# Kernel optimization log

Measured on AMD Instinct MI355X. Metric: run time of the kernel, lower is better.

## Reference

```python
import jax, jax.numpy as jnp
import numpy as np

N_NODES = 10000
N_EDGES = 320000
D_IN = 256
D_OUT = 256
NEG_SLOPE = 0.2


def setup_inputs() -> dict:
    key = jax.random.key(0)
    ks = jax.random.split(key, 8)
    feature = jax.random.normal(ks[0], (N_NODES, D_IN), dtype=jnp.float32)
    src = jax.random.randint(ks[1], (N_EDGES,), 0, N_NODES, dtype=jnp.int32)
    dst = jax.random.randint(ks[2], (N_EDGES,), 0, N_NODES, dtype=jnp.int32)
    # Xavier-ish scaled weights
    s = 1.0 / np.sqrt(D_IN)
    W_s = jax.random.normal(ks[3], (D_OUT, D_IN), dtype=jnp.float32) * s
    W_t = jax.random.normal(ks[4], (D_OUT, D_IN), dtype=jnp.float32) * s
    W_attn = jax.random.normal(ks[5], (1, D_OUT), dtype=jnp.float32) * (1.0 / np.sqrt(D_OUT))
    W_fc = jax.random.normal(ks[6], (D_OUT, D_IN), dtype=jnp.float32) * s
    b_fc = jnp.zeros((D_OUT,), dtype=jnp.float32)
    return {"feature": feature, "src": src, "dst": dst,
            "W_s": W_s, "W_t": W_t, "W_attn": W_attn,
            "W_fc": W_fc, "b_fc": b_fc}


def reference(feature, src, dst, W_s, W_t, W_attn, W_fc, b_fc):
    n = feature.shape[0]
    # Project at node level, then gather (same math as projecting gathered feats).
    proj_s = feature @ W_s.T          # [N, D_OUT]
    proj_t = feature @ W_t.T          # [N, D_OUT]
    # Edge attention logits: attn(LeakyReLU(h_dst + h_src))
    z = proj_s[src] + proj_t[dst]     # [E, D_OUT]
    z = jnp.where(z >= 0, z, NEG_SLOPE * z)
    e = (z @ W_attn.T)[:, 0]          # [E]
    # edge_softmax with norm_by='src': softmax over outgoing edges of each src node
    m = jax.ops.segment_max(e, src, num_segments=n)          # [N]
    m = jnp.where(jnp.isfinite(m), m, 0.0)                   # guard empty segments
    e_exp = jnp.exp(e - m[src])                               # [E]
    denom = jax.ops.segment_sum(e_exp, src, num_segments=n)  # [N]
    alpha = e_exp / denom[src]                                # [E]
    # message = src feature * alpha; reduce = sum at dst
    msg = feature[src] * alpha[:, None]                       # [E, D_IN]
    agg = jax.ops.segment_sum(msg, dst, num_segments=n)       # [N, D_IN]
    # final linear
    return agg @ W_fc.T + b_fc
```

## Files before the change

### kernel.cpp

```cpp
#include <hip/hip_runtime.h>
#include <math.h>

#define N_NODES 10000
#define N_EDGES 320000
#define D 256
#define NEG_SLOPE 0.2f
#define BCAP 96
#define BLOCK 256
#define NF4 (N_NODES * D / 4)
#define NW4 (256 * 256 / 4)
#define NTILE_M 157
#define NTILES (NTILE_M * 12)
#define FILL_BLOCKS ((N_EDGES + BLOCK - 1) / BLOCK)
#define CPAD 66

typedef unsigned short ushortT;
typedef __attribute__((ext_vector_type(8))) short bf16x8;
typedef __attribute__((ext_vector_type(4))) float f32x4;

__device__ __forceinline__ unsigned short f2bf(float f) {
  unsigned int u = __float_as_uint(f);
  u += 0x7FFFu + ((u >> 16) & 1u);
  return (unsigned short)(u >> 16);
}
__device__ __forceinline__ float bf2f(unsigned short u) {
  return __uint_as_float((unsigned int)u << 16);
}

typedef const __attribute__((address_space(1))) unsigned int* gas_ptr;
typedef __attribute__((address_space(3))) unsigned int* las_ptr;
__device__ __forceinline__ void gload16(const void* g, void* l) {
  __builtin_amdgcn_global_load_lds((gas_ptr)g, (las_ptr)l, 16, 0, 0);
}

__global__ void prep_kernel(const float* __restrict__ feat,
                            const float* __restrict__ Ws,
                            const float* __restrict__ Wt,
                            const float* __restrict__ Wfc,
                            ushortT* __restrict__ featb,
                            ushortT* __restrict__ Wcat,
                            int* __restrict__ cnt,
                            float* __restrict__ denom) {
  const int g = blockIdx.x * blockDim.x + threadIdx.x;
  if (g < NF4) {
    float4 v = ((const float4*)feat)[g];
    ushort4 u;
    u.x = f2bf(v.x); u.y = f2bf(v.y); u.z = f2bf(v.z); u.w = f2bf(v.w);
    ((ushort4*)featb)[g] = u;
    return;
  }
  const int gi = g - NF4;
  if (gi < 3 * NW4) {
    const float* W = (gi < NW4) ? Ws : ((gi < 2 * NW4) ? Wt : Wfc);
    const int off = gi - ((gi < NW4) ? 0 : ((gi < 2 * NW4) ? NW4 : 2 * NW4));
    float4 v = ((const float4*)W)[off];
    ushort4 u;
    u.x = f2bf(v.x); u.y = f2bf(v.y); u.z = f2bf(v.z); u.w = f2bf(v.w);
    ((ushort4*)Wcat)[gi] = u;
    return;
  }
  const int gn = gi - 3 * NW4;
  if (gn < N_NODES) {
    cnt[gn] = 0;
    denom[gn] = 0.f;
  }
}

__global__ __launch_bounds__(256, 2) void proj_fill_kernel(
    const ushortT* __restrict__ featb,
    const ushortT* __restrict__ Wcat,
    const int* __restrict__ src, const int* __restrict__ dst,
    int* __restrict__ cnt, int* __restrict__ src_b,
    ushortT* __restrict__ ps, ushortT* __restrict__ pt,
    ushortT* __restrict__ fcp) {
  __shared__ ushortT Als[64][D];
  __shared__ ushortT Bls[64][D];
  __shared__ ushortT Cls[64][CPAD];

  if (blockIdx.x < FILL_BLOCKS) {
    const int i = blockIdx.x * BLOCK + threadIdx.x;
    if (i < N_EDGES) {
      const int dn = dst[i];
      const int slot = atomicAdd(&cnt[dn], 1);
      if (slot < BCAP) src_b[dn * BCAP + slot] = src[i];
    }
    return;
  }
  const int p = blockIdx.x - FILL_BLOCKS;
  const int m0 = (p / 12) * 64;
  const int by = p % 12;
  ushortT* outp = (by < 4) ? ps : ((by < 8) ? pt : fcp);
  const int col0 = (by & 3) * 64;
  const int n0 = by * 64;

  const int tid = threadIdx.x;
  const int wave = tid >> 6;
  const int lane = tid & 63;
  const int quad = lane >> 4;
  const int l16 = lane & 15;

  const int m_base_t = (wave & 1) * 32;
  const int wn = wave >> 1;

  {
    const int rl = lane >> 5;
    const int cph = lane & 31;
#pragma unroll
    for (int c = 0; c < 8; ++c) {
      const int r = wave * 16 + c * 2 + rl;
      const int clog = cph ^ (r & 7);
      gload16(featb + (size_t)(m0 + r) * D + clog * 8, &Als[wave * 16 + c * 2][0]);
      gload16(Wcat + (size_t)(n0 + r) * D + clog * 8, &Bls[wave * 16 + c * 2][0]);
    }
  }
  __syncthreads();

  f32x4 acc[2][2];
#pragma unroll
  for (int i = 0; i < 2; ++i)
#pragma unroll
    for (int j = 0; j < 2; ++j) acc[i][j] = (f32x4){0.f, 0.f, 0.f, 0.f};

  const int ar0 = m_base_t + l16;
  const int br0 = wn * 32 + l16;
  const int xa = ar0 & 7;
  const int xb = br0 & 7;
#pragma unroll
  for (int kk = 0; kk < 8; ++kk) {
    const int j = kk * 4 + quad;
    const int ea = (j ^ xa) * 8;
    const int eb = (j ^ xb) * 8;
    bf16x8 a0 = *(const bf16x8*)&Als[ar0][ea];
    bf16x8 a1 = *(const bf16x8*)&Als[ar0 + 16][ea];
    bf16x8 b0 = *(const bf16x8*)&Bls[br0][eb];
    bf16x8 b1 = *(const bf16x8*)&Bls[br0 + 16][eb];
    acc[0][0] = __builtin_amdgcn_mfma_f32_16x16x32_bf16(a0, b0, acc[0][0], 0, 0, 0);
    acc[0][1] = __builtin_amdgcn_mfma_f32_16x16x32_bf16(a0, b1, acc[0][1], 0, 0, 0);
    acc[1][0] = __builtin_amdgcn_mfma_f32_16x16x32_bf16(a1, b0, acc[1][0], 0, 0, 0);
    acc[1][1] = __builtin_amdgcn_mfma_f32_16x16x32_bf16(a1, b1, acc[1][1], 0, 0, 0);
  }

#pragma unroll
  for (int mi = 0; mi < 2; ++mi)
#pragma unroll
    for (int r = 0; r < 4; ++r) {
      const int row = m_base_t + mi * 16 + quad * 4 + r;
#pragma unroll
      for (int ni = 0; ni < 2; ++ni)
        Cls[row][wn * 32 + ni * 16 + l16] = f2bf(acc[mi][ni][r]);
    }
  __syncthreads();
#pragma unroll
  for (int it = 0; it < 2; ++it) {
    const int idx = tid + it * 256;
    const int row = idx >> 3;
    const int cc = (idx & 7) * 8;
    const int grow = m0 + row;
    if (grow < N_NODES)
      *(bf16x8*)(outp + (size_t)grow * D + col0 + cc) = *(const bf16x8*)&Cls[row][cc];
  }
}

__global__ __launch_bounds__(256) void logit_bucket_kernel(
    const ushortT* __restrict__ ps,
    const ushortT* __restrict__ pt,
    const int* __restrict__ cnt,
    const int* __restrict__ src_b,
    const float* __restrict__ Wattn,
    float* __restrict__ expv_b,
    float* __restrict__ denom) {
  const int wave = threadIdx.x >> 6;
  const int n = blockIdx.x * 4 + wave;
  if (n >= N_NODES) return;
  const int cn = min(cnt[n], BCAP);
  if (cn == 0) return;
  const int lane = threadIdx.x & 63;
  const int half = lane >> 5;
  const int l32 = lane & 31;
  const int base = n * BCAP;

  bf16x8 bu = *(const bf16x8*)(pt + (size_t)n * D + l32 * 8);
  float b[8], w[8];
  const float4 w0 = *(const float4*)(Wattn + l32 * 8);
  const float4 w1 = *(const float4*)(Wattn + l32 * 8 + 4);
  w[0] = w0.x; w[1] = w0.y; w[2] = w0.z; w[3] = w0.w;
  w[4] = w1.x; w[5] = w1.y; w[6] = w1.z; w[7] = w1.w;
#pragma unroll
  for (int i = 0; i < 8; ++i) b[i] = bf2f((unsigned short)bu[i]);

  int j = half;
  for (; j + 6 < cn; j += 8) {
    const int s0 = src_b[base + j];
    const int s1 = src_b[base + j + 2];
    const int s2 = src_b[base + j + 4];
    const int s3 = src_b[base + j + 6];
    bf16x8 au0 = *(const bf16x8*)(ps + (size_t)s0 * D + l32 * 8);
    bf16x8 au1 = *(const bf16x8*)(ps + (size_t)s1 * D + l32 * 8);
    bf16x8 au2 = *(const bf16x8*)(ps + (size_t)s2 * D + l32 * 8);
    bf16x8 au3 = *(const bf16x8*)(ps + (size_t)s3 * D + l32 * 8);
    float sum0 = 0.f, sum1 = 0.f, sum2 = 0.f, sum3 = 0.f;
#pragma unroll
    for (int i = 0; i < 8; ++i) {
      float z0 = bf2f((unsigned short)au0[i]) + b[i];
      float z1 = bf2f((unsigned short)au1[i]) + b[i];
      float z2 = bf2f((unsigned short)au2[i]) + b[i];
      float z3 = bf2f((unsigned short)au3[i]) + b[i];
      z0 = fmaxf(z0, NEG_SLOPE * z0);
      z1 = fmaxf(z1, NEG_SLOPE * z1);
      z2 = fmaxf(z2, NEG_SLOPE * z2);
      z3 = fmaxf(z3, NEG_SLOPE * z3);
      sum0 = fmaf(w[i], z0, sum0);
      sum1 = fmaf(w[i], z1, sum1);
      sum2 = fmaf(w[i], z2, sum2);
      sum3 = fmaf(w[i], z3, sum3);
    }
#pragma unroll
    for (int off = 16; off > 0; off >>= 1) {
      sum0 += __shfl_down(sum0, off, 32);
      sum1 += __shfl_down(sum1, off, 32);
      sum2 += __shfl_down(sum2, off, 32);
      sum3 += __shfl_down(sum3, off, 32);
    }
    if (l32 == 0) {
      float ex0 = __expf(sum0), ex1 = __expf(sum1);
      float ex2 = __expf(sum2), ex3 = __expf(sum3);
      expv_b[base + j] = ex0;
      expv_b[base + j + 2] = ex1;
      expv_b[base + j + 4] = ex2;
      expv_b[base + j + 6] = ex3;
      atomicAdd(&denom[s0], ex0);
      atomicAdd(&denom[s1], ex1);
      atomicAdd(&denom[s2], ex2);
      atomicAdd(&denom[s3], ex3);
    }
  }
  for (; j < cn; j += 2) {
    const int s = src_b[base + j];
    bf16x8 au = *(const bf16x8*)(ps + (size_t)s * D + l32 * 8);
    float sum = 0.f;
#pragma unroll
    for (int i = 0; i < 8; ++i) {
      float z = bf2f((unsigned short)au[i]) + b[i];
      z = fmaxf(z, NEG_SLOPE * z);
      sum = fmaf(w[i], z, sum);
    }
#pragma unroll
    for (int off = 16; off > 0; off >>= 1) sum += __shfl_down(sum, off, 32);
    if (l32 == 0) {
      float ex = __expf(sum);
      expv_b[base + j] = ex;
      atomicAdd(&denom[s], ex);
    }
  }
}

__global__ __launch_bounds__(256) void gather_agg_kernel(
    const ushortT* __restrict__ fcp,
    const int* __restrict__ cnt,
    const int* __restrict__ src_b,
    const float* __restrict__ expv_b,
    const float* __restrict__ denom,
    const float* __restrict__ b_fc,
    float* __restrict__ out) {
  const int wave = threadIdx.x >> 6;
  const int n = blockIdx.x * 4 + wave;
  if (n >= N_NODES) return;
  const int lane = threadIdx.x & 63;
  const int half = lane >> 5;
  const int l32 = lane & 31;
  const int cn = min(cnt[n], BCAP);
  const int base = n * BCAP;

  float acc[8];
#pragma unroll
  for (int i = 0; i < 8; ++i) acc[i] = 0.f;

  int j = half;
  for (; j + 6 < cn; j += 8) {
    const int s0 = src_b[base + j];
    const int s1 = src_b[base + j + 2];
    const int s2 = src_b[base + j + 4];
    const int s3 = src_b[base + j + 6];
    const float a0 = expv_b[base + j] / denom[s0];
    const float a1 = expv_b[base + j + 2] / denom[s1];
    const float a2 = expv_b[base + j + 4] / denom[s2];
    const float a3 = expv_b[base + j + 6] / denom[s3];
    bf16x8 f0 = *(const bf16x8*)(fcp + (size_t)s0 * D + l32 * 8);
    bf16x8 f1 = *(const bf16x8*)(fcp + (size_t)s1 * D + l32 * 8);
    bf16x8 f2 = *(const bf16x8*)(fcp + (size_t)s2 * D + l32 * 8);
    bf16x8 f3 = *(const bf16x8*)(fcp + (size_t)s3 * D + l32 * 8);
#pragma unroll
    for (int i = 0; i < 8; ++i) {
      acc[i] = fmaf(a0, bf2f((unsigned short)f0[i]), acc[i]);
      acc[i] = fmaf(a1, bf2f((unsigned short)f1[i]), acc[i]);
      acc[i] = fmaf(a2, bf2f((unsigned short)f2[i]), acc[i]);
      acc[i] = fmaf(a3, bf2f((unsigned short)f3[i]), acc[i]);
    }
  }
  for (; j < cn; j += 2) {
    const int s = src_b[base + j];
    const float a = expv_b[base + j] / denom[s];
    bf16x8 fu = *(const bf16x8*)(fcp + (size_t)s * D + l32 * 8);
#pragma unroll
    for (int i = 0; i < 8; ++i)
      acc[i] = fmaf(a, bf2f((unsigned short)fu[i]), acc[i]);
  }
#pragma unroll
  for (int i = 0; i < 8; ++i) acc[i] += __shfl_xor(acc[i], 32);
  if (half == 0) {
    const float4 bf0 = *(const float4*)(b_fc + l32 * 8);
    const float4 bf1 = *(const float4*)(b_fc + l32 * 8 + 4);
    float4 o0 = make_float4(acc[0] + bf0.x, acc[1] + bf0.y, acc[2] + bf0.z, acc[3] + bf0.w);
    float4 o1 = make_float4(acc[4] + bf1.x, acc[5] + bf1.y, acc[6] + bf1.z, acc[7] + bf1.w);
    *(float4*)(out + (size_t)n * D + l32 * 8) = o0;
    *(float4*)(out + (size_t)n * D + l32 * 8 + 4) = o1;
  }
}

extern "C" void kernel_launch(void* const* d_in, const int* in_sizes, int n_in,
                              void* d_out, int out_size, void* d_ws, size_t ws_size,
                              hipStream_t stream) {
  const float* feat  = (const float*)d_in[0];
  const int*   src   = (const int*)d_in[1];
  const int*   dst   = (const int*)d_in[2];
  const float* Ws    = (const float*)d_in[3];
  const float* Wt    = (const float*)d_in[4];
  const float* Wattn = (const float*)d_in[5];
  const float* Wfc   = (const float*)d_in[6];
  const float* bfc   = (const float*)d_in[7];
  float* out = (float*)d_out;

  ushortT* ps    = (ushortT*)d_ws;
  ushortT* pt    = ps + (size_t)N_NODES * D;
  ushortT* fcp   = pt + (size_t)N_NODES * D;
  ushortT* featb = fcp + (size_t)N_NODES * D;
  ushortT* Wcat  = featb + (size_t)N_NODES * D;
  float* expv_b  = (float*)(Wcat + (size_t)768 * 256);
  float* denom   = expv_b + (size_t)N_NODES * BCAP;
  int*   cnt     = (int*)(denom + N_NODES);
  int*   src_b   = cnt + N_NODES;

  const int prep_items = NF4 + 3 * NW4 + N_NODES;
  const int nodeblocks = (N_NODES + 3) / 4;
  prep_kernel<<<(prep_items + BLOCK - 1) / BLOCK, BLOCK, 0, stream>>>(
      feat, Ws, Wt, Wfc, featb, Wcat, cnt, denom);
  proj_fill_kernel<<<FILL_BLOCKS + NTILES, BLOCK, 0, stream>>>(
      featb, Wcat, src, dst, cnt, src_b, ps, pt, fcp);
  logit_bucket_kernel<<<nodeblocks, BLOCK, 0, stream>>>(ps, pt, cnt, src_b, Wattn, expv_b, denom);
  gather_agg_kernel<<<nodeblocks, BLOCK, 0, stream>>>(fcp, cnt, src_b, expv_b, denom, bfc, out);
}
```

Baseline: 162.1 us.

## Quantize gathered projection rows to int8 with per-row scales

```diff
diff --git a/kernel.cpp b/kernel.cpp
--- a/kernel.cpp
+++ b/kernel.cpp
@@ -25,6 +25,9 @@
 }
 __device__ __forceinline__ float bf2f(unsigned short u) {
   return __uint_as_float((unsigned int)u << 16);
+}
+__device__ __forceinline__ float i8get(int w, int i) {
+  return (float)((signed char)(w >> (8 * i)));
 }
 
 typedef const __attribute__((address_space(1))) unsigned int* gas_ptr;
@@ -161,8 +164,37 @@
   }
 }
 
+__global__ __launch_bounds__(256) void quant_kernel(
+    const ushortT* __restrict__ ps, const ushortT* __restrict__ fcp,
+    signed char* __restrict__ ps8, signed char* __restrict__ fcp8,
+    float* __restrict__ sps, float* __restrict__ sfcp) {
+  const int wid = blockIdx.x * 4 + (threadIdx.x >> 6);
+  if (wid >= 2 * N_NODES) return;
+  const int lane = threadIdx.x & 63;
+  const bool isPs = (wid < N_NODES);
+  const int row = isPs ? wid : wid - N_NODES;
+  const ushortT* sp = isPs ? ps : fcp;
+  signed char* dp = isPs ? ps8 : fcp8;
+  float* scp = isPs ? sps : sfcp;
+
+  ushort4 u = *(const ushort4*)(sp + (size_t)row * D + lane * 4);
+  float v0 = bf2f(u.x), v1 = bf2f(u.y), v2 = bf2f(u.z), v3 = bf2f(u.w);
+  float m = fmaxf(fmaxf(fabsf(v0), fabsf(v1)), fmaxf(fabsf(v2), fabsf(v3)));
+#pragma unroll
+  for (int off = 32; off > 0; off >>= 1) m = fmaxf(m, __shfl_xor(m, off));
+  const float rs = (m > 0.f) ? 127.f / m : 0.f;
+  const int q0 = (int)rintf(v0 * rs);
+  const int q1 = (int)rintf(v1 * rs);
+  const int q2 = (int)rintf(v2 * rs);
+  const int q3 = (int)rintf(v3 * rs);
+  const int packed = (q0 & 255) | ((q1 & 255) << 8) | ((q2 & 255) << 16) | (q3 << 24);
+  ((int*)dp)[row * 64 + lane] = packed;
+  if (lane == 0) scp[row] = m * (1.f / 127.f);
+}
+
 __global__ __launch_bounds__(256) void logit_bucket_kernel(
-    const ushortT* __restrict__ ps,
+    const signed char* __restrict__ ps8,
+    const float* __restrict__ sps,
     const ushortT* __restrict__ pt,
     const int* __restrict__ cnt,
     const int* __restrict__ src_b,
@@ -194,17 +226,23 @@
     const int s1 = src_b[base + j + 2];
     const int s2 = src_b[base + j + 4];
     const int s3 = src_b[base + j + 6];
-    bf16x8 au0 = *(const bf16x8*)(ps + (size_t)s0 * D + l32 * 8);
-    bf16x8 au1 = *(const bf16x8*)(ps + (size_t)s1 * D + l32 * 8);
-    bf16x8 au2 = *(const bf16x8*)(ps + (size_t)s2 * D + l32 * 8);
-    bf16x8 au3 = *(const bf16x8*)(ps + (size_t)s3 * D + l32 * 8);
+    const int2 q0 = *(const int2*)(ps8 + (size_t)s0 * D + l32 * 8);
+    const int2 q1 = *(const int2*)(ps8 + (size_t)s1 * D + l32 * 8);
+    const int2 q2 = *(const int2*)(ps8 + (size_t)s2 * D + l32 * 8);
+    const int2 q3 = *(const int2*)(ps8 + (size_t)s3 * D + l32 * 8);
+    const float c0 = sps[s0], c1 = sps[s1], c2 = sps[s2], c3 = sps[s3];
     float sum0 = 0.f, sum1 = 0.f, sum2 = 0.f, sum3 = 0.f;
 #pragma unroll
     for (int i = 0; i < 8; ++i) {
-      float z0 = bf2f((unsigned short)au0[i]) + b[i];
-      float z1 = bf2f((unsigned short)au1[i]) + b[i];
-      float z2 = bf2f((unsigned short)au2[i]) + b[i];
-      float z3 = bf2f((unsigned short)au3[i]) + b[i];
+      const int w0q = (i < 4) ? q0.x : q0.y;
+      const int w1q = (i < 4) ? q1.x : q1.y;
+      const int w2q = (i < 4) ? q2.x : q2.y;
+      const int w3q = (i < 4) ? q3.x : q3.y;
+      const int bi = i & 3;
+      float z0 = fmaf(i8get(w0q, bi), c0, b[i]);
+      float z1 = fmaf(i8get(w1q, bi), c1, b[i]);
+      float z2 = fmaf(i8get(w2q, bi), c2, b[i]);
+      float z3 = fmaf(i8get(w3q, bi), c3, b[i]);
       z0 = fmaxf(z0, NEG_SLOPE * z0);
       z1 = fmaxf(z1, NEG_SLOPE * z1);
       z2 = fmaxf(z2, NEG_SLOPE * z2);
@@ -236,11 +274,13 @@
   }
   for (; j < cn; j += 2) {
     const int s = src_b[base + j];
-    bf16x8 au = *(const bf16x8*)(ps + (size_t)s * D + l32 * 8);
+    const int2 q = *(const int2*)(ps8 + (size_t)s * D + l32 * 8);
+    const float c = sps[s];
     float sum = 0.f;
 #pragma unroll
     for (int i = 0; i < 8; ++i) {
-      float z = bf2f((unsigned short)au[i]) + b[i];
+      const int wq = (i < 4) ? q.x : q.y;
+      float z = fmaf(i8get(wq, i & 3), c, b[i]);
       z = fmaxf(z, NEG_SLOPE * z);
       sum = fmaf(w[i], z, sum);
     }
@@ -255,7 +295,8 @@
 }
 
 __global__ __launch_bounds__(256) void gather_agg_kernel(
-    const ushortT* __restrict__ fcp,
+    const signed char* __restrict__ fcp8,
+    const float* __restrict__ sfcp,
     const int* __restrict__ cnt,
     const int* __restrict__ src_b,
     const float* __restrict__ expv_b,
@@ -281,29 +322,30 @@
     const int s1 = src_b[base + j + 2];
     const int s2 = src_b[base + j + 4];
     const int s3 = src_b[base + j + 6];
-    const float a0 = expv_b[base + j] / denom[s0];
-    const float a1 = expv_b[base + j + 2] / denom[s1];
-    const float a2 = expv_b[base + j + 4] / denom[s2];
-    const float a3 = expv_b[base + j + 6] / denom[s3];
-    bf16x8 f0 = *(const bf16x8*)(fcp + (size_t)s0 * D + l32 * 8);
-    bf16x8 f1 = *(const bf16x8*)(fcp + (size_t)s1 * D + l32 * 8);
-    bf16x8 f2 = *(const bf16x8*)(fcp + (size_t)s2 * D + l32 * 8);
-    bf16x8 f3 = *(const bf16x8*)(fcp + (size_t)s3 * D + l32 * 8);
+    const float a0 = expv_b[base + j] / denom[s0] * sfcp[s0];
+    const float a1 = expv_b[base + j + 2] / denom[s1] * sfcp[s1];
+    const float a2 = expv_b[base + j + 4] / denom[s2] * sfcp[s2];
+    const float a3 = expv_b[base + j + 6] / denom[s3] * sfcp[s3];
+    const int2 q0 = *(const int2*)(fcp8 + (size_t)s0 * D + l32 * 8);
+    const int2 q1 = *(const int2*)(fcp8 + (size_t)s1 * D + l32 * 8);
+    const int2 q2 = *(const int2*)(fcp8 + (size_t)s2 * D + l32 * 8);
+    const int2 q3 = *(const int2*)(fcp8 + (size_t)s3 * D + l32 * 8);
 #pragma unroll
     for (int i = 0; i < 8; ++i) {
-      acc[i] = fmaf(a0, bf2f((unsigned short)f0[i]), acc[i]);
-      acc[i] = fmaf(a1, bf2f((unsigned short)f1[i]), acc[i]);
-      acc[i] = fmaf(a2, bf2f((unsigned short)f2[i]), acc[i]);
-      acc[i] = fmaf(a3, bf2f((unsigned short)f3[i]), acc[i]);
+      const int bi = i & 3;
+      acc[i] = fmaf(a0, i8get((i < 4) ? q0.x : q0.y, bi), acc[i]);
+      acc[i] = fmaf(a1, i8get((i < 4) ? q1.x : q1.y, bi), acc[i]);
+      acc[i] = fmaf(a2, i8get((i < 4) ? q2.x : q2.y, bi), acc[i]);
+      acc[i] = fmaf(a3, i8get((i < 4) ? q3.x : q3.y, bi), acc[i]);
     }
   }
   for (; j < cn; j += 2) {
     const int s = src_b[base + j];
-    const float a = expv_b[base + j] / denom[s];
-    bf16x8 fu = *(const bf16x8*)(fcp + (size_t)s * D + l32 * 8);
+    const float a = expv_b[base + j] / denom[s] * sfcp[s];
+    const int2 q = *(const int2*)(fcp8 + (size_t)s * D + l32 * 8);
 #pragma unroll
     for (int i = 0; i < 8; ++i)
-      acc[i] = fmaf(a, bf2f((unsigned short)fu[i]), acc[i]);
+      acc[i] = fmaf(a, i8get((i < 4) ? q.x : q.y, i & 3), acc[i]);
   }
 #pragma unroll
   for (int i = 0; i < 8; ++i) acc[i] += __shfl_xor(acc[i], 32);
@@ -339,6 +381,10 @@
   float* denom   = expv_b + (size_t)N_NODES * BCAP;
   int*   cnt     = (int*)(denom + N_NODES);
   int*   src_b   = cnt + N_NODES;
+  signed char* ps8  = (signed char*)(src_b + (size_t)N_NODES * BCAP);
+  signed char* fcp8 = ps8 + (size_t)N_NODES * D;
+  float* sps     = (float*)(fcp8 + (size_t)N_NODES * D);
+  float* sfcp    = sps + N_NODES;
 
   const int prep_items = NF4 + 3 * NW4 + N_NODES;
   const int nodeblocks = (N_NODES + 3) / 4;
@@ -346,6 +392,7 @@
       feat, Ws, Wt, Wfc, featb, Wcat, cnt, denom);
   proj_fill_kernel<<<FILL_BLOCKS + NTILES, BLOCK, 0, stream>>>(
       featb, Wcat, src, dst, cnt, src_b, ps, pt, fcp);
-  logit_bucket_kernel<<<nodeblocks, BLOCK, 0, stream>>>(ps, pt, cnt, src_b, Wattn, expv_b, denom);
-  gather_agg_kernel<<<nodeblocks, BLOCK, 0, stream>>>(fcp, cnt, src_b, expv_b, denom, bfc, out);
-}
+  quant_kernel<<<(2 * N_NODES + 3) / 4, BLOCK, 0, stream>>>(ps, fcp, ps8, fcp8, sps, sfcp);
+  logit_bucket_kernel<<<nodeblocks, BLOCK, 0, stream>>>(ps8, sps, pt, cnt, src_b, Wattn, expv_b, denom);
+  gather_agg_kernel<<<nodeblocks, BLOCK, 0, stream>>>(fcp8, sfcp, cnt, src_b, expv_b, denom, bfc, out);
+}
```

Result: slower. 166.7 us (+2.8%).

## Merge four kernels into one persistent cooperative kernel with grid syncs

Applied to the files above, without the earlier changes.

```diff
diff --git a/kernel.cpp b/kernel.cpp
--- a/kernel.cpp
+++ b/kernel.cpp
@@ -1,5 +1,8 @@
 #include <hip/hip_runtime.h>
+#include <hip/hip_cooperative_groups.h>
 #include <math.h>
+
+namespace cg = cooperative_groups;
 
 #define N_NODES 10000
 #define N_EDGES 320000
@@ -11,8 +14,8 @@
 #define NW4 (256 * 256 / 4)
 #define NTILE_M 157
 #define NTILES (NTILE_M * 12)
-#define FILL_BLOCKS ((N_EDGES + BLOCK - 1) / BLOCK)
 #define CPAD 66
+#define PREP_ITEMS (NF4 + 3 * NW4 + N_NODES)
 
 typedef unsigned short ushortT;
 typedef __attribute__((ext_vector_type(8))) short bf16x8;
@@ -33,287 +36,274 @@
   __builtin_amdgcn_global_load_lds((gas_ptr)g, (las_ptr)l, 16, 0, 0);
 }
 
-__global__ void prep_kernel(const float* __restrict__ feat,
-                            const float* __restrict__ Ws,
-                            const float* __restrict__ Wt,
-                            const float* __restrict__ Wfc,
-                            ushortT* __restrict__ featb,
-                            ushortT* __restrict__ Wcat,
-                            int* __restrict__ cnt,
-                            float* __restrict__ denom) {
-  const int g = blockIdx.x * blockDim.x + threadIdx.x;
-  if (g < NF4) {
-    float4 v = ((const float4*)feat)[g];
-    ushort4 u;
-    u.x = f2bf(v.x); u.y = f2bf(v.y); u.z = f2bf(v.z); u.w = f2bf(v.w);
-    ((ushort4*)featb)[g] = u;
-    return;
-  }
-  const int gi = g - NF4;
-  if (gi < 3 * NW4) {
-    const float* W = (gi < NW4) ? Ws : ((gi < 2 * NW4) ? Wt : Wfc);
-    const int off = gi - ((gi < NW4) ? 0 : ((gi < 2 * NW4) ? NW4 : 2 * NW4));
-    float4 v = ((const float4*)W)[off];
-    ushort4 u;
-    u.x = f2bf(v.x); u.y = f2bf(v.y); u.z = f2bf(v.z); u.w = f2bf(v.w);
-    ((ushort4*)Wcat)[gi] = u;
-    return;
-  }
-  const int gn = gi - 3 * NW4;
-  if (gn < N_NODES) {
-    cnt[gn] = 0;
-    denom[gn] = 0.f;
-  }
-}
-
-__global__ __launch_bounds__(256, 2) void proj_fill_kernel(
-    const ushortT* __restrict__ featb,
-    const ushortT* __restrict__ Wcat,
-    const int* __restrict__ src, const int* __restrict__ dst,
-    int* __restrict__ cnt, int* __restrict__ src_b,
+__global__ __launch_bounds__(256, 2) void mega_kernel(
+    const float* __restrict__ feat, const int* __restrict__ src,
+    const int* __restrict__ dst, const float* __restrict__ Ws,
+    const float* __restrict__ Wt, const float* __restrict__ Wattn,
+    const float* __restrict__ Wfc, const float* __restrict__ bfc,
+    ushortT* __restrict__ featb, ushortT* __restrict__ Wcat,
     ushortT* __restrict__ ps, ushortT* __restrict__ pt,
-    ushortT* __restrict__ fcp) {
+    ushortT* __restrict__ fcp, float* __restrict__ expv_b,
+    float* __restrict__ denom, int* __restrict__ cnt,
+    int* __restrict__ src_b, float* __restrict__ out) {
   __shared__ ushortT Als[64][D];
   __shared__ ushortT Bls[64][D];
   __shared__ ushortT Cls[64][CPAD];
 
-  if (blockIdx.x < FILL_BLOCKS) {
-    const int i = blockIdx.x * BLOCK + threadIdx.x;
-    if (i < N_EDGES) {
-      const int dn = dst[i];
-      const int slot = atomicAdd(&cnt[dn], 1);
-      if (slot < BCAP) src_b[dn * BCAP + slot] = src[i];
+  cg::grid_group grid = cg::this_grid();
+  const int tid = threadIdx.x;
+  const int gtid = blockIdx.x * BLOCK + tid;
+  const int gthreads = gridDim.x * BLOCK;
+
+  for (int g = gtid; g < PREP_ITEMS; g += gthreads) {
+    if (g < NF4) {
+      float4 v = ((const float4*)feat)[g];
+      ushort4 u;
+      u.x = f2bf(v.x); u.y = f2bf(v.y); u.z = f2bf(v.z); u.w = f2bf(v.w);
+      ((ushort4*)featb)[g] = u;
+    } else {
+      const int gi = g - NF4;
+      if (gi < 3 * NW4) {
+        const float* W = (gi < NW4) ? Ws : ((gi < 2 * NW4) ? Wt : Wfc);
+        const int off = gi - ((gi < NW4) ? 0 : ((gi < 2 * NW4) ? NW4 : 2 * NW4));
+        float4 v = ((const float4*)W)[off];
+        ushort4 u;
+        u.x = f2bf(v.x); u.y = f2bf(v.y); u.z = f2bf(v.z); u.w = f2bf(v.w);
+        ((ushort4*)Wcat)[gi] = u;
+      } else {
+        const int gn = gi - 3 * NW4;
+        if (gn < N_NODES) { cnt[gn] = 0; denom[gn] = 0.f; }
+      }
     }
-    return;
-  }
-  const int p = blockIdx.x - FILL_BLOCKS;
-  const int m0 = (p / 12) * 64;
-  const int by = p % 12;
-  ushortT* outp = (by < 4) ? ps : ((by < 8) ? pt : fcp);
-  const int col0 = (by & 3) * 64;
-  const int n0 = by * 64;
-
-  const int tid = threadIdx.x;
-  const int wave = tid >> 6;
-  const int lane = tid & 63;
-  const int quad = lane >> 4;
-  const int l16 = lane & 15;
-
-  const int m_base_t = (wave & 1) * 32;
-  const int wn = wave >> 1;
-
+  }
+  __threadfence();
+  grid.sync();
+
+  for (int i = gtid; i < N_EDGES; i += gthreads) {
+    const int dn = dst[i];
+    const int slot = atomicAdd(&cnt[dn], 1);
+    if (slot < BCAP) src_b[dn * BCAP + slot] = src[i];
+  }
   {
+    const int wave = tid >> 6;
+    const int lane = tid & 63;
+    const int quad = lane >> 4;
+    const int l16 = lane & 15;
+    const int m_base_t = (wave & 1) * 32;
+    const int wn = wave >> 1;
     const int rl = lane >> 5;
     const int cph = lane & 31;
-#pragma unroll
-    for (int c = 0; c < 8; ++c) {
-      const int r = wave * 16 + c * 2 + rl;
-      const int clog = cph ^ (r & 7);
-      gload16(featb + (size_t)(m0 + r) * D + clog * 8, &Als[wave * 16 + c * 2][0]);
-      gload16(Wcat + (size_t)(n0 + r) * D + clog * 8, &Bls[wave * 16 + c * 2][0]);
+    const int ar0 = m_base_t + l16;
+    const int br0 = wn * 32 + l16;
+    const int xa = ar0 & 7;
+    const int xb = br0 & 7;
+
+    for (int p = blockIdx.x; p < NTILES; p += gridDim.x) {
+      const int m0 = (p / 12) * 64;
+      const int by = p % 12;
+      ushortT* outp = (by < 4) ? ps : ((by < 8) ? pt : fcp);
+      const int col0 = (by & 3) * 64;
+      const int n0 = by * 64;
+
+#pragma unroll
+      for (int c = 0; c < 8; ++c) {
+        const int r = wave * 16 + c * 2 + rl;
+        const int clog = cph ^ (r & 7);
+        gload16(featb + (size_t)(m0 + r) * D + clog * 8, &Als[wave * 16 + c * 2][0]);
+        gload16(Wcat + (size_t)(n0 + r) * D + clog * 8, &Bls[wave * 16 + c * 2][0]);
+      }
+      __syncthreads();
+
+      f32x4 acc[2][2];
+#pragma unroll
+      for (int i2 = 0; i2 < 2; ++i2)
+#pragma unroll
+        for (int j2 = 0; j2 < 2; ++j2) acc[i2][j2] = (f32x4){0.f, 0.f, 0.f, 0.f};
+
+#pragma unroll
+      for (int kk = 0; kk < 8; ++kk) {
+        const int j = kk * 4 + quad;
+        const int ea = (j ^ xa) * 8;
+        const int eb = (j ^ xb) * 8;
+        bf16x8 a0 = *(const bf16x8*)&Als[ar0][ea];
+        bf16x8 a1 = *(const bf16x8*)&Als[ar0 + 16][ea];
+        bf16x8 b0 = *(const bf16x8*)&Bls[br0][eb];
+        bf16x8 b1 = *(const bf16x8*)&Bls[br0 + 16][eb];
+        acc[0][0] = __builtin_amdgcn_mfma_f32_16x16x32_bf16(a0, b0, acc[0][0], 0, 0, 0);
+        acc[0][1] = __builtin_amdgcn_mfma_f32_16x16x32_bf16(a0, b1, acc[0][1], 0, 0, 0);
+        acc[1][0] = __builtin_amdgcn_mfma_f32_16x16x32_bf16(a1, b0, acc[1][0], 0, 0, 0);
+        acc[1][1] = __builtin_amdgcn_mfma_f32_16x16x32_bf16(a1, b1, acc[1][1], 0, 0, 0);
+      }
+
+#pragma unroll
+      for (int mi = 0; mi < 2; ++mi)
+#pragma unroll
+        for (int r = 0; r < 4; ++r) {
+          const int row = m_base_t + mi * 16 + quad * 4 + r;
+#pragma unroll
+          for (int ni = 0; ni < 2; ++ni)
+            Cls[row][wn * 32 + ni * 16 + l16] = f2bf(acc[mi][ni][r]);
+        }
+      __syncthreads();
+#pragma unroll
+      for (int it = 0; it < 2; ++it) {
+        const int idx = tid + it * 256;
+        const int row = idx >> 3;
+        const int cc = (idx & 7) * 8;
+        const int grow = m0 + row;
+        if (grow < N_NODES)
+          *(bf16x8*)(outp + (size_t)grow * D + col0 + cc) = *(const bf16x8*)&Cls[row][cc];
+      }
     }
   }
-  __syncthreads();
-
-  f32x4 acc[2][2];
-#pragma unroll
-  for (int i = 0; i < 2; ++i)
-#pragma unroll
-    for (int j = 0; j < 2; ++j) acc[i][j] = (f32x4){0.f, 0.f, 0.f, 0.f};
-
-  const int ar0 = m_base_t + l16;
-  const int br0 = wn * 32 + l16;
-  const int xa = ar0 & 7;
-  const int xb = br0 & 7;
-#pragma unroll
-  for (int kk = 0; kk < 8; ++kk) {
-    const int j = kk * 4 + quad;
-    const int ea = (j ^ xa) * 8;
-    const int eb = (j ^ xb) * 8;
-    bf16x8 a0 = *(const bf16x8*)&Als[ar0][ea];
-    bf16x8 a1 = *(const bf16x8*)&Als[ar0 + 16][ea];
-    bf16x8 b0 = *(const bf16x8*)&Bls[br0][eb];
-    bf16x8 b1 = *(const bf16x8*)&Bls[br0 + 16][eb];
-    acc[0][0] = __builtin_amdgcn_mfma_f32_16x16x32_bf16(a0, b0, acc[0][0], 0, 0, 0);
-    acc[0][1] = __builtin_amdgcn_mfma_f32_16x16x32_bf16(a0, b1, acc[0][1], 0, 0, 0);
-    acc[1][0] = __builtin_amdgcn_mfma_f32_16x16x32_bf16(a1, b0, acc[1][0], 0, 0, 0);
-    acc[1][1] = __builtin_amdgcn_mfma_f32_16x16x32_bf16(a1, b1, acc[1][1], 0, 0, 0);
-  }
-
-#pragma unroll
-  for (int mi = 0; mi < 2; ++mi)
-#pragma unroll
-    for (int r = 0; r < 4; ++r) {
-      const int row = m_base_t + mi * 16 + quad * 4 + r;
-#pragma unroll
-      for (int ni = 0; ni < 2; ++ni)
-        Cls[row][wn * 32 + ni * 16 + l16] = f2bf(acc[mi][ni][r]);
+  __threadfence();
+  grid.sync();
+
+  {
+    const int gwave = gtid >> 6;
+    const int nwaves = gthreads >> 6;
+    const int lane = tid & 63;
+    const int half = lane >> 5;
+    const int l32 = lane & 31;
+    float w[8];
+    const float4 w0 = *(const float4*)(Wattn + l32 * 8);
+    const float4 w1 = *(const float4*)(Wattn + l32 * 8 + 4);
+    w[0] = w0.x; w[1] = w0.y; w[2] = w0.z; w[3] = w0.w;
+    w[4] = w1.x; w[5] = w1.y; w[6] = w1.z; w[7] = w1.w;
+
+    for (int n = gwave; n < N_NODES; n += nwaves) {
+      const int cn = min(cnt[n], BCAP);
+      if (cn == 0) continue;
+      const int base = n * BCAP;
+      bf16x8 bu = *(const bf16x8*)(pt + (size_t)n * D + l32 * 8);
+      float b[8];
+#pragma unroll
+      for (int i = 0; i < 8; ++i) b[i] = bf2f((unsigned short)bu[i]);
+
+      int j = half;
+      for (; j + 6 < cn; j += 8) {
+        const int s0 = src_b[base + j];
+        const int s1 = src_b[base + j + 2];
+        const int s2 = src_b[base + j + 4];
+        const int s3 = src_b[base + j + 6];
+        bf16x8 au0 = *(const bf16x8*)(ps + (size_t)s0 * D + l32 * 8);
+        bf16x8 au1 = *(const bf16x8*)(ps + (size_t)s1 * D + l32 * 8);
+        bf16x8 au2 = *(const bf16x8*)(ps + (size_t)s2 * D + l32 * 8);
+        bf16x8 au3 = *(const bf16x8*)(ps + (size_t)s3 * D + l32 * 8);
+        float sum0 = 0.f, sum1 = 0.f, sum2 = 0.f, sum3 = 0.f;
+#pragma unroll
+        for (int i = 0; i < 8; ++i) {
+          float z0 = bf2f((unsigned short)au0[i]) + b[i];
+          float z1 = bf2f((unsigned short)au1[i]) + b[i];
+          float z2 = bf2f((unsigned short)au2[i]) + b[i];
+          float z3 = bf2f((unsigned short)au3[i]) + b[i];
+          z0 = fmaxf(z0, NEG_SLOPE * z0);
+          z1 = fmaxf(z1, NEG_SLOPE * z1);
+          z2 = fmaxf(z2, NEG_SLOPE * z2);
+          z3 = fmaxf(z3, NEG_SLOPE * z3);
+          sum0 = fmaf(w[i], z0, sum0);
+          sum1 = fmaf(w[i], z1, sum1);
+          sum2 = fmaf(w[i], z2, sum2);
+          sum3 = fmaf(w[i], z3, sum3);
+        }
+#pragma unroll
+        for (int off = 16; off > 0; off >>= 1) {
+          sum0 += __shfl_down(sum0, off, 32);
+          sum1 += __shfl_down(sum1, off, 32);
+          sum2 += __shfl_down(sum2, off, 32);
+          sum3 += __shfl_down(sum3, off, 32);
+        }
+        if (l32 == 0) {
+          float ex0 = __expf(sum0), ex1 = __expf(sum1);
+          float ex2 = __expf(sum2), ex3 = __expf(sum3);
+          expv_b[base + j] = ex0;
+          expv_b[base + j + 2] = ex1;
+          expv_b[base + j + 4] = ex2;
+          expv_b[base + j + 6] = ex3;
+          atomicAdd(&denom[s0], ex0);
+          atomicAdd(&denom[s1], ex1);
+          atomicAdd(&denom[s2], ex2);
+          atomicAdd(&denom[s3], ex3);
+        }
+      }
+      for (; j < cn; j += 2) {
+        const int s = src_b[base + j];
+        bf16x8 au = *(const bf16x8*)(ps + (size_t)s * D + l32 * 8);
+        float sum = 0.f;
+#pragma unroll
+        for (int i = 0; i < 8; ++i) {
+          float z = bf2f((unsigned short)au[i]) + b[i];
+          z = fmaxf(z, NEG_SLOPE * z);
+          sum = fmaf(w[i], z, sum);
+        }
+#pragma unroll
+        for (int off = 16; off > 0; off >>= 1) sum += __shfl_down(sum, off, 32);
+        if (l32 == 0) {
+          float ex = __expf(sum);
+          expv_b[base + j] = ex;
+          atomicAdd(&denom[s], ex);
+        }
+      }
     }
-  __syncthreads();
-#pragma unroll
-  for (int it = 0; it < 2; ++it) {
-    const int idx = tid + it * 256;
-    const int row = idx >> 3;
-    const int cc = (idx & 7) * 8;
-    const int grow = m0 + row;
-    if (grow < N_NODES)
-      *(bf16x8*)(outp + (size_t)grow * D + col0 + cc) = *(const bf16x8*)&Cls[row][cc];
-  }
-}
-
-__global__ __launch_bounds__(256) void logit_bucket_kernel(
-    const ushortT* __restrict__ ps,
-    const ushortT* __restrict__ pt,
-    const int* __restrict__ cnt,
-    const int* __restrict__ src_b,
-    const float* __restrict__ Wattn,
-    float* __restrict__ expv_b,
-    float* __restrict__ denom) {
-  const int wave = threadIdx.x >> 6;
-  const int n = blockIdx.x * 4 + wave;
-  if (n >= N_NODES) return;
-  const int cn = min(cnt[n], BCAP);
-  if (cn == 0) return;
-  const int lane = threadIdx.x & 63;
-  const int half = lane >> 5;
-  const int l32 = lane & 31;
-  const int base = n * BCAP;
-
-  bf16x8 bu = *(const bf16x8*)(pt + (size_t)n * D + l32 * 8);
-  float b[8], w[8];
-  const float4 w0 = *(const float4*)(Wattn + l32 * 8);
-  const float4 w1 = *(const float4*)(Wattn + l32 * 8 + 4);
-  w[0] = w0.x; w[1] = w0.y; w[2] = w0.z; w[3] = w0.w;
-  w[4] = w1.x; w[5] = w1.y; w[6] = w1.z; w[7] = w1.w;
-#pragma unroll
-  for (int i = 0; i < 8; ++i) b[i] = bf2f((unsigned short)bu[i]);
-
-  int j = half;
-  for (; j + 6 < cn; j += 8) {
-    const int s0 = src_b[base + j];
-    const int s1 = src_b[base + j + 2];
-    const int s2 = src_b[base + j + 4];
-    const int s3 = src_b[base + j + 6];
-    bf16x8 au0 = *(const bf16x8*)(ps + (size_t)s0 * D + l32 * 8);
-    bf16x8 au1 = *(const bf16x8*)(ps + (size_t)s1 * D + l32 * 8);
-    bf16x8 au2 = *(const bf16x8*)(ps + (size_t)s2 * D + l32 * 8);
-    bf16x8 au3 = *(const bf16x8*)(ps + (size_t)s3 * D + l32 * 8);
-    float sum0 = 0.f, sum1 = 0.f, sum2 = 0.f, sum3 = 0.f;
-#pragma unroll
-    for (int i = 0; i < 8; ++i) {
-      float z0 = bf2f((unsigned short)au0[i]) + b[i];
-      float z1 = bf2f((unsigned short)au1[i]) + b[i];
-      float z2 = bf2f((unsigned short)au2[i]) + b[i];
-      float z3 = bf2f((unsigned short)au3[i]) + b[i];
-      z0 = fmaxf(z0, NEG_SLOPE * z0);
-      z1 = fmaxf(z1, NEG_SLOPE * z1);
-      z2 = fmaxf(z2, NEG_SLOPE * z2);
-      z3 = fmaxf(z3, NEG_SLOPE * z3);
-      sum0 = fmaf(w[i], z0, sum0);
-      sum1 = fmaf(w[i], z1, sum1);
-      sum2 = fmaf(w[i], z2, sum2);
-      sum3 = fmaf(w[i], z3, sum3);
+  }
+  __threadfence();
+  grid.sync();
+
+  {
+    const int gwave = gtid >> 6;
+    const int nwaves = gthreads >> 6;
+    const int lane = tid & 63;
+    const int half = lane >> 5;
+    const int l32 = lane & 31;
+
+    for (int n = gwave; n < N_NODES; n += nwaves) {
+      const int cn = min(cnt[n], BCAP);
+      const int base = n * BCAP;
+      float acc[8];
+#pragma unroll
+      for (int i = 0; i < 8; ++i) acc[i] = 0.f;
+
+      int j = half;
+      for (; j + 6 < cn; j += 8) {
+        const int s0 = src_b[base + j];
+        const int s1 = src_b[base + j + 2];
+        const int s2 = src_b[base + j + 4];
+        const int s3 = src_b[base + j + 6];
+        const float a0 = expv_b[base + j] / denom[s0];
+        const float a1 = expv_b[base + j + 2] / denom[s1];
+        const float a2 = expv_b[base + j + 4] / denom[s2];
+        const float a3 = expv_b[base + j + 6] / denom[s3];
+        bf16x8 f0 = *(const bf16x8*)(fcp + (size_t)s0 * D + l32 * 8);
+        bf16x8 f1 = *(const bf16x8*)(fcp + (size_t)s1 * D + l32 * 8);
+        bf16x8 f2 = *(const bf16x8*)(fcp + (size_t)s2 * D + l32 * 8);
+        bf16x8 f3 = *(const bf16x8*)(fcp + (size_t)s3 * D + l32 * 8);
+#pragma unroll
+        for (int i = 0; i < 8; ++i) {
+          acc[i] = fmaf(a0, bf2f((unsigned short)f0[i]), acc[i]);
+          acc[i] = fmaf(a1, bf2f((unsigned short)f1[i]), acc[i]);
+          acc[i] = fmaf(a2, bf2f((unsigned short)f2[i]), acc[i]);
+          acc[i] = fmaf(a3, bf2f((unsigned short)f3[i]), acc[i]);
+        }
+      }
+      for (; j < cn; j += 2) {
+        const int s = src_b[base + j];
+        const float a = expv_b[base + j] / denom[s];
+        bf16x8 fu = *(const bf16x8*)(fcp + (size_t)s * D + l32 * 8);
+#pragma unroll
+        for (int i = 0; i < 8; ++i)
+          acc[i] = fmaf(a, bf2f((unsigned short)fu[i]), acc[i]);
+      }
+#pragma unroll
+      for (int i = 0; i < 8; ++i) acc[i] += __shfl_xor(acc[i], 32);
+      if (half == 0) {
+        const float4 bf0 = *(const float4*)(bfc + l32 * 8);
+        const float4 bf1 = *(const float4*)(bfc + l32 * 8 + 4);
+        float4 o0 = make_float4(acc[0] + bf0.x, acc[1] + bf0.y, acc[2] + bf0.z, acc[3] + bf0.w);
+        float4 o1 = make_float4(acc[4] + bf1.x, acc[5] + bf1.y, acc[6] + bf1.z, acc[7] + bf1.w);
+        *(float4*)(out + (size_t)n * D + l32 * 8) = o0;
+        *(float4*)(out + (size_t)n * D + l32 * 8 + 4) = o1;
+      }
     }
-#pragma unroll
-    for (int off = 16; off > 0; off >>= 1) {
-      sum0 += __shfl_down(sum0, off, 32);
-      sum1 += __shfl_down(sum1, off, 32);
-      sum2 += __shfl_down(sum2, off, 32);
-      sum3 += __shfl_down(sum3, off, 32);
-    }
-    if (l32 == 0) {
-      float ex0 = __expf(sum0), ex1 = __expf(sum1);
-      float ex2 = __expf(sum2), ex3 = __expf(sum3);
-      expv_b[base + j] = ex0;
-      expv_b[base + j + 2] = ex1;
-      expv_b[base + j + 4] = ex2;
-      expv_b[base + j + 6] = ex3;
-      atomicAdd(&denom[s0], ex0);
-      atomicAdd(&denom[s1], ex1);
-      atomicAdd(&denom[s2], ex2);
-      atomicAdd(&denom[s3], ex3);
-    }
-  }
-  for (; j < cn; j += 2) {
-    const int s = src_b[base + j];
-    bf16x8 au = *(const bf16x8*)(ps + (size_t)s * D + l32 * 8);
-    float sum = 0.f;
-#pragma unroll
-    for (int i = 0; i < 8; ++i) {
-      float z = bf2f((unsigned short)au[i]) + b[i];
-      z = fmaxf(z, NEG_SLOPE * z);
-      sum = fmaf(w[i], z, sum);
-    }
-#pragma unroll
-    for (int off = 16; off > 0; off >>= 1) sum += __shfl_down(sum, off, 32);
-    if (l32 == 0) {
-      float ex = __expf(sum);
-      expv_b[base + j] = ex;
-      atomicAdd(&denom[s], ex);
-    }
-  }
-}
-
-__global__ __launch_bounds__(256) void gather_agg_kernel(
-    const ushortT* __restrict__ fcp,
-    const int* __restrict__ cnt,
-    const int* __restrict__ src_b,
-    const float* __restrict__ expv_b,
-    const float* __restrict__ denom,
-    const float* __restrict__ b_fc,
-    float* __restrict__ out) {
-  const int wave = threadIdx.x >> 6;
-  const int n = blockIdx.x * 4 + wave;
-  if (n >= N_NODES) return;
-  const int lane = threadIdx.x & 63;
-  const int half = lane >> 5;
-  const int l32 = lane & 31;
-  const int cn = min(cnt[n], BCAP);
-  const int base = n * BCAP;
-
-  float acc[8];
-#pragma unroll
-  for (int i = 0; i < 8; ++i) acc[i] = 0.f;
-
-  int j = half;
-  for (; j + 6 < cn; j += 8) {
-    const int s0 = src_b[base + j];
-    const int s1 = src_b[base + j + 2];
-    const int s2 = src_b[base + j + 4];
-    const int s3 = src_b[base + j + 6];
-    const float a0 = expv_b[base + j] / denom[s0];
-    const float a1 = expv_b[base + j + 2] / denom[s1];
-    const float a2 = expv_b[base + j + 4] / denom[s2];
-    const float a3 = expv_b[base + j + 6] / denom[s3];
-    bf16x8 f0 = *(const bf16x8*)(fcp + (size_t)s0 * D + l32 * 8);
-    bf16x8 f1 = *(const bf16x8*)(fcp + (size_t)s1 * D + l32 * 8);
-    bf16x8 f2 = *(const bf16x8*)(fcp + (size_t)s2 * D + l32 * 8);
-    bf16x8 f3 = *(const bf16x8*)(fcp + (size_t)s3 * D + l32 * 8);
-#pragma unroll
-    for (int i = 0; i < 8; ++i) {
-      acc[i] = fmaf(a0, bf2f((unsigned short)f0[i]), acc[i]);
-      acc[i] = fmaf(a1, bf2f((unsigned short)f1[i]), acc[i]);
-      acc[i] = fmaf(a2, bf2f((unsigned short)f2[i]), acc[i]);
-      acc[i] = fmaf(a3, bf2f((unsigned short)f3[i]), acc[i]);
-    }
-  }
-  for (; j < cn; j += 2) {
-    const int s = src_b[base + j];
-    const float a = expv_b[base + j] / denom[s];
-    bf16x8 fu = *(const bf16x8*)(fcp + (size_t)s * D + l32 * 8);
-#pragma unroll
-    for (int i = 0; i < 8; ++i)
-      acc[i] = fmaf(a, bf2f((unsigned short)fu[i]), acc[i]);
-  }
-#pragma unroll
-  for (int i = 0; i < 8; ++i) acc[i] += __shfl_xor(acc[i], 32);
-  if (half == 0) {
-    const float4 bf0 = *(const float4*)(b_fc + l32 * 8);
-    const float4 bf1 = *(const float4*)(b_fc + l32 * 8 + 4);
-    float4 o0 = make_float4(acc[0] + bf0.x, acc[1] + bf0.y, acc[2] + bf0.z, acc[3] + bf0.w);
-    float4 o1 = make_float4(acc[4] + bf1.x, acc[5] + bf1.y, acc[6] + bf1.z, acc[7] + bf1.w);
-    *(float4*)(out + (size_t)n * D + l32 * 8) = o0;
-    *(float4*)(out + (size_t)n * D + l32 * 8 + 4) = o1;
   }
 }
 
@@ -340,12 +330,17 @@
   int*   cnt     = (int*)(denom + N_NODES);
   int*   src_b   = cnt + N_NODES;
 
-  const int prep_items = NF4 + 3 * NW4 + N_NODES;
-  const int nodeblocks = (N_NODES + 3) / 4;
-  prep_kernel<<<(prep_items + BLOCK - 1) / BLOCK, BLOCK, 0, stream>>>(
-      feat, Ws, Wt, Wfc, featb, Wcat, cnt, denom);
-  proj_fill_kernel<<<FILL_BLOCKS + NTILES, BLOCK, 0, stream>>>(
-      featb, Wcat, src, dst, cnt, src_b, ps, pt, fcp);
-  logit_bucket_kernel<<<nodeblocks, BLOCK, 0, stream>>>(ps, pt, cnt, src_b, Wattn, expv_b, denom);
-  gather_agg_kernel<<<nodeblocks, BLOCK, 0, stream>>>(fcp, cnt, src_b, expv_b, denom, bfc, out);
-}
+  int nb = 2;
+  hipOccupancyMaxActiveBlocksPerMultiprocessor(&nb, mega_kernel, BLOCK, 0);
+  if (nb < 1) nb = 1;
+  int gridsz = nb * 256;
+  if (gridsz > 1024) gridsz = 1024;
+
+  void* args[] = {(void*)&feat, (void*)&src, (void*)&dst, (void*)&Ws, (void*)&Wt,
+                  (void*)&Wattn, (void*)&Wfc, (void*)&bfc, (void*)&featb,
+                  (void*)&Wcat, (void*)&ps, (void*)&pt, (void*)&fcp,
+                  (void*)&expv_b, (void*)&denom, (void*)&cnt, (void*)&src_b,
+                  (void*)&out};
+  hipLaunchCooperativeKernel((void*)mega_kernel, dim3(gridsz), dim3(BLOCK),
+                             args, 0, stream);
+}
```

Measured after the change: 481.4 us. 2.97x slower.
